# Kernel optimization log

Measured on AMD Instinct MI355X. Metric: run time of the kernel, lower is better.

## Reference

```python
import jax, jax.numpy as jnp
import numpy as np

K = 3       # kernel_size
RATE = 2    # dilation rate
NH = 8      # num_heads
EPS = 1e-5  # InstanceNorm eps


def _conv1x1(x, W, b):
    # x: [B,C,H,W], W: [O,C], b: [O]
    return jnp.einsum('bchw,oc->bohw', x, W) + b[None, :, None, None]


def _inorm(x):
    mu = jnp.mean(x, axis=(2, 3), keepdims=True)
    var = jnp.var(x, axis=(2, 3), keepdims=True)
    return (x - mu) / jnp.sqrt(var + EPS)


def _extract_patches(x):
    # dilated KxK patches, stride 1, 'same' grid -> [B, C, K*K, H, W]
    B, C, H, W = x.shape
    pad = RATE * (K - 1) // 2
    xp = jnp.pad(x, ((0, 0), (0, 0), (pad, pad), (pad, pad)))
    taps = [xp[:, :, i * RATE:i * RATE + H, j * RATE:j * RATE + W]
            for i in range(K) for j in range(K)]
    return jnp.stack(taps, axis=2)


def setup_inputs() -> dict:
    key = jax.random.key(0)
    ks = jax.random.split(key, 8)
    B, C, H, W, A = 1, 64, 64, 64, 128
    features = jax.random.normal(ks[0], (B, C, H, W), jnp.float32)
    masks = jax.random.uniform(ks[1], (B, 1, H, W), jnp.float32)
    s_in = 1.0 / np.sqrt(C).astype(np.float32)
    Wq = jax.random.normal(ks[2], (A, C), jnp.float32) * s_in
    bq = jnp.zeros((A,), jnp.float32)
    Wk = jax.random.normal(ks[3], (A, C), jnp.float32) * s_in
    bk = jnp.zeros((A,), jnp.float32)
    Wo = jax.random.normal(ks[4], (C, C), jnp.float32) * s_in
    bo = jnp.zeros((C,), jnp.float32)
    return dict(features=features, masks=masks, Wq=Wq, bq=bq,
                Wk=Wk, bk=bk, Wo=Wo, bo=bo)


def reference(features, masks, Wq, bq, Wk, bk, Wo, bo):
    B, C, H, W = features.shape
    A = Wq.shape[0]
    hc = A // NH
    L = H * W
    KK = K * K

    m = (masks > 0.5).astype(features.dtype)          # 1 = hole
    f_masked = features * m
    f_unmasked = features * (1.0 - m)

    q = jax.nn.relu(_inorm(_conv1x1(f_masked, Wq, bq)))    # [B,A,H,W]
    k = jax.nn.relu(_inorm(_conv1x1(f_unmasked, Wk, bk)))  # [B,A,H,W]

    # per-head dilated patch banks: [B,NH,hc*KK,L]
    qp = _extract_patches(q).reshape(B, NH, hc * KK, L)
    kp = _extract_patches(k).reshape(B, NH, hc * KK, L)

    # patch-correlation attention per head: [B,NH,L,L]
    attn = jax.nn.softmax(jnp.einsum('bndq,bndk->bnqk', qp, kp), axis=-1)

    # value patch bank from unmasked features: [B,C*KK,L]
    vp = _extract_patches(f_unmasked).reshape(B, C * KK, L)

    # sample value patches: [B,NH,L,C*KK]
    sampled = jnp.einsum('bnqk,bdk->bnqd', attn, vp)

    # fold: average the KK taps per channel, then average over heads
    attended = sampled.reshape(B, NH, L, C, KK).mean(axis=4).mean(axis=1)  # [B,L,C]
    attended = attended.transpose(0, 2, 1).reshape(B, C, H, W)

    return jax.nn.relu(_inorm(_conv1x1(attended, Wo, bo)))
```

## Files before the change

### kernel.cpp

```cpp
#include <hip/hip_runtime.h>
#include <hip/hip_bf16.h>


#define LL 4096
#define CC 64
#define AA 128
#define NH_ 8
#define KSTR 144
#define LOG2E 1.44269504088896340736f

typedef _Float16 half8 __attribute__((ext_vector_type(8)));
typedef float floatx4 __attribute__((ext_vector_type(4)));
typedef int intx4 __attribute__((ext_vector_type(4)));

__device__ __forceinline__ float fexp2(float x) {
    float r;
    asm("v_exp_f32 %0, %1" : "=v"(r) : "v"(x));
    return r;
}

__global__ __launch_bounds__(512) void prep_kernel(
    const float* __restrict__ feat,
    const float* __restrict__ masks,
    const float* __restrict__ Wq, const float* __restrict__ bq,
    const float* __restrict__ Wk, const float* __restrict__ bk,
    _Float16* __restrict__ q_act, _Float16* __restrict__ k_act,
    _Float16* __restrict__ vb)
{
    const int tid = threadIdx.x;
    const int b = blockIdx.x;
    __shared__ float sW[CC];
    __shared__ float sm[16];

    if (b >= 2 * AA) {
        int c = b - 2 * AA;
        for (int p = 0; p < 8; ++p) {
            int l = p * 512 + tid;
            int y = l >> 6, x = l & 63;
            float s = 0.f;
            for (int ty = 0; ty < 3; ++ty) {
                int yy = y + 2 * (ty - 1);
                if (yy < 0 || yy > 63) continue;
                for (int tx = 0; tx < 3; ++tx) {
                    int xx = x + 2 * (tx - 1);
                    if (xx < 0 || xx > 63) continue;
                    int ll = yy * 64 + xx;
                    float hole = masks[ll] > 0.5f ? 1.f : 0.f;
                    s += feat[c * LL + ll] * (1.f - hole);
                }
            }
            vb[c * LL + l] = (_Float16)(s * (1.f / 9.f));
        }
        return;
    }

    const int a = b & (AA - 1);
    const int sel = b >> 7;
    const float* Wrow = (sel ? Wk : Wq) + a * CC;
    const float bias = sel ? bk[a] : bq[a];
    if (tid < CC) sW[tid] = Wrow[tid];
    __syncthreads();

    float acc[8];
#pragma unroll
    for (int p = 0; p < 8; ++p) acc[p] = 0.f;
    for (int c = 0; c < CC; ++c) {
        float wc = sW[c];
        const float* fr = feat + (size_t)c * LL + tid;
#pragma unroll
        for (int p = 0; p < 8; ++p) acc[p] += wc * fr[p * 512];
    }

    float vals[8];
    float s1 = 0.f, s2 = 0.f;
#pragma unroll
    for (int p = 0; p < 8; ++p) {
        int l = p * 512 + tid;
        float hole = masks[l] > 0.5f ? 1.f : 0.f;
        float mf = sel ? (1.f - hole) : hole;
        float v = acc[p] * mf + bias;
        vals[p] = v; s1 += v; s2 += v * v;
    }
    for (int off = 32; off; off >>= 1) {
        s1 += __shfl_down(s1, off, 64);
        s2 += __shfl_down(s2, off, 64);
    }
    int wv = tid >> 6, ln = tid & 63;
    if (ln == 0) { sm[wv * 2] = s1; sm[wv * 2 + 1] = s2; }
    __syncthreads();
    s1 = 0.f; s2 = 0.f;
#pragma unroll
    for (int i = 0; i < 8; ++i) { s1 += sm[2 * i]; s2 += sm[2 * i + 1]; }
    float mu = s1 * (1.f / LL);
    float inv = rsqrtf(s2 * (1.f / LL) - mu * mu + 1e-5f);

    const float oscale = sel ? 1.f : LOG2E;
    _Float16* act = (sel ? k_act : q_act) + (size_t)a * LL;
#pragma unroll
    for (int p = 0; p < 8; ++p) {
        int l = p * 512 + tid;
        float v = (vals[p] - mu) * inv;
        act[l] = (_Float16)(v > 0.f ? v * oscale : 0.f);
    }
}

__global__ __launch_bounds__(256) void build_kp(
    const _Float16* __restrict__ k_act, _Float16* __restrict__ kp)
{
    const int n = blockIdx.x, y = blockIdx.y;
    const int tid = threadIdx.x;
    const _Float16* ka = k_act + (size_t)n * 16 * LL;
    __shared__ _Float16 kt[16][3][72];

    for (int idx = tid; idx < 16 * 3 * 68; idx += 256) {
        int row = idx / 68, xr = idx - row * 68;
        int ah = row / 3, ty = row - ah * 3;
        int yy = y + 2 * (ty - 1);
        int xx = xr - 2;
        _Float16 v = (_Float16)0.f;
        if (yy >= 0 && yy <= 63 && xx >= 0 && xx <= 63)
            v = ka[ah * LL + yy * 64 + xx];
        kt[ah][ty][xr] = v;
    }
    __syncthreads();

    _Float16* base = kp + ((size_t)n * LL + y * 64) * KSTR;
#pragma unroll
    for (int i = 0; i < 5; ++i) {
        int idx = tid + i * 256;
        if (idx < 64 * 18) {
            int x = idx / 18, c18 = idx - x * 18;
            half8 v8;
#pragma unroll
            for (int j = 0; j < 8; ++j) {
                int d = c18 * 8 + j;
                int ah = d / 9, t = d - ah * 9;
                int ty = t / 3, tx = t - ty * 3;
                v8[j] = kt[ah][ty][x + 2 * tx];
            }
            *(half8*)(base + (size_t)idx * 8) = v8;
        }
    }
}

__global__ __launch_bounds__(256, 2) void attn_kernel(
    const _Float16* __restrict__ q_act, const _Float16* __restrict__ kp,
    const _Float16* __restrict__ vb,
    _Float16* __restrict__ Opart, float* __restrict__ ml)
{
    const int bid = blockIdx.x;
    const int n = bid & 7;
    const int slot = bid >> 3;
    const int qt2 = slot & 31;
    const int h = slot >> 5;
    const int jt0 = h * 32;
    const int tid = threadIdx.x;
    const int w = tid >> 6, lane = tid & 63;
    const int l15 = lane & 15, quad = lane >> 4;

    __shared__ __align__(16) _Float16 Bk[2][64 * KSTR + 16];

    if (tid < 32) Bk[tid >> 4][64 * KSTR + (tid & 15)] = (_Float16)0.f;

    const _Float16* kpn = kp + (size_t)n * LL * KSTR;

    auto issue_bk = [&](int jt, _Float16* dst) {
        const char* tile = (const char*)(kpn + (size_t)jt * 64 * KSTR) + (lane << 4);
        for (int c = w; c < 18; c += 4) {
            __builtin_amdgcn_global_load_lds(
                (const __attribute__((address_space(1))) void*)(tile + c * 1024),
                (__attribute__((address_space(3))) void*)(dst + c * 512),
                16, 0, 0);
        }
    };

    half8 afrag[2][5];
    {
        const _Float16* qa = q_act + (size_t)n * 16 * LL;
        const int x = w * 16 + l15;
#pragma unroll
        for (int rs = 0; rs < 2; ++rs) {
            const int y = qt2 * 2 + rs;
#pragma unroll
            for (int ks = 0; ks < 5; ++ks) {
#pragma unroll
                for (int j = 0; j < 8; ++j) {
                    int d = ks * 32 + quad * 8 + j;
                    _Float16 v = (_Float16)0.f;
                    if (d < 144) {
                        int ah = d / 9, t = d - ah * 9;
                        int ty = t / 3, tx = t - ty * 3;
                        int yy = y + 2 * (ty - 1);
                        int xx = x + 2 * (tx - 1);
                        if (yy >= 0 && yy <= 63 && xx >= 0 && xx <= 63)
                            v = qa[ah * LL + yy * 64 + xx];
                    }
                    afrag[rs][ks][j] = v;
                }
            }
        }
    }

    floatx4 accO[2][4];
    float mrow[2], lrow[2];
#pragma unroll
    for (int rs = 0; rs < 2; ++rs) {
        mrow[rs] = -1e30f; lrow[rs] = 0.f;
#pragma unroll
        for (int i = 0; i < 4; ++i) accO[rs][i] = (floatx4){0.f, 0.f, 0.f, 0.f};
    }

    const int aLo = (((quad & 1) << 5) + l15) << 2;
    const int aHi = aLo + 64;
    const bool selHi = (quad >> 1) != 0;

    const _Float16* vpl = vb + (size_t)l15 * LL + quad * 8;

    auto softmax_pack = [&](floatx4* accS, floatx4* accOr,
                            float& mr, float& lr, half8* pfr) {
        float t0 = fmaxf(fmaxf(accS[0][0], accS[0][1]), fmaxf(accS[0][2], accS[0][3]));
        float t1 = fmaxf(fmaxf(accS[1][0], accS[1][1]), fmaxf(accS[1][2], accS[1][3]));
        float t2 = fmaxf(fmaxf(accS[2][0], accS[2][1]), fmaxf(accS[2][2], accS[2][3]));
        float t3 = fmaxf(fmaxf(accS[3][0], accS[3][1]), fmaxf(accS[3][2], accS[3][3]));
        float tm = fmaxf(fmaxf(t0, t1), fmaxf(t2, t3));
        tm = fmaxf(tm, __shfl_xor(tm, 16, 64));
        tm = fmaxf(tm, __shfl_xor(tm, 32, 64));
        float mn = fmaxf(mr, tm);
        float alpha = fexp2(mr - mn);
        mr = mn;
        lr *= alpha;
        float af[4];
#pragma unroll
        for (int r = 0; r < 4; ++r) af[r] = __shfl(alpha, quad * 4 + r, 16);
#pragma unroll
        for (int nt = 0; nt < 4; ++nt)
#pragma unroll
            for (int r = 0; r < 4; ++r) accOr[nt][r] *= af[r];
        float rsum = 0.f;
#pragma unroll
        for (int nt = 0; nt < 4; ++nt)
#pragma unroll
            for (int r = 0; r < 4; ++r) {
                float pv = fexp2(accS[nt][r] - mn);
                accS[nt][r] = pv;
                rsum += pv;
            }
        lr += rsum;

        int pkw[4][2];
#pragma unroll
        for (int nt = 0; nt < 4; ++nt)
#pragma unroll
            for (int rp = 0; rp < 2; ++rp) {
                auto hp = __builtin_amdgcn_cvt_pkrtz(accS[nt][2 * rp],
                                                     accS[nt][2 * rp + 1]);
                pkw[nt][rp] = __builtin_bit_cast(int, hp);
            }
#pragma unroll
        for (int ks2 = 0; ks2 < 2; ++ks2) {
            int w0A = __builtin_amdgcn_ds_bpermute(aLo, pkw[2 * ks2][0]);
            int w0B = __builtin_amdgcn_ds_bpermute(aLo, pkw[2 * ks2 + 1][0]);
            int w1A = __builtin_amdgcn_ds_bpermute(aLo, pkw[2 * ks2][1]);
            int w1B = __builtin_amdgcn_ds_bpermute(aLo, pkw[2 * ks2 + 1][1]);
            int w2A = __builtin_amdgcn_ds_bpermute(aHi, pkw[2 * ks2][0]);
            int w2B = __builtin_amdgcn_ds_bpermute(aHi, pkw[2 * ks2 + 1][0]);
            int w3A = __builtin_amdgcn_ds_bpermute(aHi, pkw[2 * ks2][1]);
            int w3B = __builtin_amdgcn_ds_bpermute(aHi, pkw[2 * ks2 + 1][1]);
            intx4 wvv;
            wvv[0] = selHi ? w0B : w0A;
            wvv[1] = selHi ? w1B : w1A;
            wvv[2] = selHi ? w2B : w2A;
            wvv[3] = selHi ? w3B : w3A;
            pfr[ks2] = __builtin_bit_cast(half8, wvv);
        }
    };

    issue_bk(jt0, Bk[0]);

    int cur = 0;
    for (int it = 0; it < 32; ++it) {
        __syncthreads();

        if (it < 31) issue_bk(jt0 + it + 1, Bk[cur ^ 1]);

        const _Float16* vp = vpl + (jt0 + it) * 64;
        half8 vfrag[4][2];
#pragma unroll
        for (int nt = 0; nt < 4; ++nt)
#pragma unroll
            for (int ks2 = 0; ks2 < 2; ++ks2)
                vfrag[nt][ks2] = *(const half8*)(vp + (size_t)nt * 16 * LL + ks2 * 32);

        const _Float16* bk = Bk[cur];

        floatx4 accS0[4], accS1[4];
#pragma unroll
        for (int i = 0; i < 4; ++i) {
            accS0[i] = (floatx4){0.f, 0.f, 0.f, 0.f};
            accS1[i] = (floatx4){0.f, 0.f, 0.f, 0.f};
        }
        for (int ks = 0; ks < 5; ++ks) {
#pragma unroll
            for (int nt = 0; nt < 4; ++nt) {
                half8 bfr = *(const half8*)(bk + (nt * 16 + l15) * KSTR + ks * 32 + quad * 8);
                accS0[nt] = __builtin_amdgcn_mfma_f32_16x16x32_f16(bfr, afrag[0][ks], accS0[nt], 0, 0, 0);
                accS1[nt] = __builtin_amdgcn_mfma_f32_16x16x32_f16(bfr, afrag[1][ks], accS1[nt], 0, 0, 0);
            }
        }

        half8 pfr0[2], pfr1[2];
        softmax_pack(accS0, accO[0], mrow[0], lrow[0], pfr0);
#pragma unroll
        for (int ks2 = 0; ks2 < 2; ++ks2)
#pragma unroll
            for (int nt = 0; nt < 4; ++nt)
                accO[0][nt] = __builtin_amdgcn_mfma_f32_16x16x32_f16(pfr0[ks2], vfrag[nt][ks2], accO[0][nt], 0, 0, 0);

        softmax_pack(accS1, accO[1], mrow[1], lrow[1], pfr1);
#pragma unroll
        for (int ks2 = 0; ks2 < 2; ++ks2)
#pragma unroll
            for (int nt = 0; nt < 4; ++nt)
                accO[1][nt] = __builtin_amdgcn_mfma_f32_16x16x32_f16(pfr1[ks2], vfrag[nt][ks2], accO[1][nt], 0, 0, 0);

        cur ^= 1;
    }

#pragma unroll
    for (int rs = 0; rs < 2; ++rs) {
        const int y = qt2 * 2 + rs;
        float rsum = lrow[rs];
        rsum += __shfl_xor(rsum, 16, 64);
        rsum += __shfl_xor(rsum, 32, 64);
        float invl = 1.f / rsum;
        float iv[4];
#pragma unroll
        for (int r = 0; r < 4; ++r) iv[r] = __shfl(invl, quad * 4 + r, 16);

        _Float16* op = Opart + ((size_t)(n * 2 + h) * LL + y * 64 + w * 16) * CC;
#pragma unroll
        for (int r = 0; r < 4; ++r)
#pragma unroll
            for (int nt = 0; nt < 4; ++nt)
                op[(quad * 4 + r) * CC + nt * 16 + l15] = (_Float16)(accO[rs][nt][r] * iv[r]);

        if (quad == 0) {
            float* mlp = ml + ((size_t)n * LL + y * 64 + w * 16 + l15) * 4;
            mlp[2 * h] = mrow[rs];
            mlp[2 * h + 1] = rsum;
        }
    }
}

__global__ __launch_bounds__(256) void combine_kernel(
    const _Float16* __restrict__ Opart, const float* __restrict__ ml,
    float* __restrict__ att)
{
    int t = blockIdx.x * 256 + threadIdx.x;
    int l = t >> 6, c = t & 63;
    float s = 0.f;
#pragma unroll
    for (int n = 0; n < NH_; ++n) {
        const float* mlp = ml + ((size_t)n * LL + l) * 4;
        float m0 = mlp[0], l0 = mlp[1], m1 = mlp[2], l1 = mlp[3];
        float M = fmaxf(m0, m1);
        float w0 = l0 * fexp2(m0 - M);
        float w1 = l1 * fexp2(m1 - M);
        float o0 = (float)Opart[((size_t)(2 * n) * LL + l) * CC + c];
        float o1 = (float)Opart[((size_t)(2 * n + 1) * LL + l) * CC + c];
        s += (w0 * o0 + w1 * o1) / (w0 + w1);
    }
    att[t] = s * 0.125f;
}

__global__ __launch_bounds__(1024) void out_kernel(
    const float* __restrict__ att,
    const float* __restrict__ Wo, const float* __restrict__ bo,
    float* __restrict__ out)
{
    const int o = blockIdx.x;
    const int tid = threadIdx.x;
    __shared__ float sW[CC];
    __shared__ float sm[32];
    if (tid < CC) sW[tid] = Wo[o * CC + tid];
    __syncthreads();
    const float bias = bo[o];

    float vals[4], s1 = 0.f, s2 = 0.f;
#pragma unroll
    for (int p = 0; p < 4; ++p) {
        int l = p * 1024 + tid;
        const float4* arow = (const float4*)(att + (size_t)l * CC);
        float acc = bias;
#pragma unroll
        for (int c4 = 0; c4 < 16; ++c4) {
            float4 a4 = arow[c4];
            acc += sW[c4 * 4] * a4.x + sW[c4 * 4 + 1] * a4.y +
                   sW[c4 * 4 + 2] * a4.z + sW[c4 * 4 + 3] * a4.w;
        }
        vals[p] = acc; s1 += acc; s2 += acc * acc;
    }
    for (int off = 32; off; off >>= 1) {
        s1 += __shfl_down(s1, off, 64);
        s2 += __shfl_down(s2, off, 64);
    }
    int wv = tid >> 6, ln = tid & 63;
    if (ln == 0) { sm[wv * 2] = s1; sm[wv * 2 + 1] = s2; }
    __syncthreads();
    s1 = 0.f; s2 = 0.f;
#pragma unroll
    for (int i = 0; i < 16; ++i) { s1 += sm[2 * i]; s2 += sm[2 * i + 1]; }
    float mu = s1 * (1.f / LL);
    float inv = rsqrtf(s2 * (1.f / LL) - mu * mu + 1e-5f);
#pragma unroll
    for (int p = 0; p < 4; ++p) {
        int l = p * 1024 + tid;
        float v = (vals[p] - mu) * inv;
        out[(size_t)o * LL + l] = v > 0.f ? v : 0.f;
    }
}

extern "C" void kernel_launch(void* const* d_in, const int* in_sizes, int n_in,
                              void* d_out, int out_size, void* d_ws, size_t ws_size,
                              hipStream_t stream) {
    const float* feat  = (const float*)d_in[0];
    const float* masks = (const float*)d_in[1];
    const float* Wq    = (const float*)d_in[2];
    const float* bq    = (const float*)d_in[3];
    const float* Wk    = (const float*)d_in[4];
    const float* bk    = (const float*)d_in[5];
    const float* Wo    = (const float*)d_in[6];
    const float* bo    = (const float*)d_in[7];
    float* out = (float*)d_out;

    char* ws = (char*)d_ws;
    _Float16* q_act = (_Float16*)ws;
    _Float16* k_act = (_Float16*)(ws + 1048576);
    _Float16* vb    = (_Float16*)(ws + 2097152);
    float*    att   = (float*)(ws + 2621440);
    _Float16* kp    = (_Float16*)(ws + 3670016);
    _Float16* Opart = (_Float16*)(ws + 13107200);
    float*    ml    = (float*)(ws + 21495808);

    prep_kernel<<<2 * AA + CC, 512, 0, stream>>>(feat, masks, Wq, bq, Wk, bk,
                                                 q_act, k_act, vb);
    dim3 gb(NH_, 64);
    build_kp<<<gb, 256, 0, stream>>>(k_act, kp);
    attn_kernel<<<512, 256, 0, stream>>>(q_act, kp, vb, Opart, ml);
    combine_kernel<<<LL * CC / 256, 256, 0, stream>>>(Opart, ml, att);
    out_kernel<<<CC, 1024, 0, stream>>>(att, Wo, bo, out);
}
```

Before: 228.5 us.

## Process one query row per block to double grid and raise occupancy

The attention kernel now handles a single query row per block instead of two. This halves the register footprint for A fragments, accumulators and softmax state, and raises the launch-bounds occupancy hint from 2 to 4 blocks. The grid doubles to 1024 blocks. In exchange, each K tile loaded into LDS and each V fragment read from global memory is reused by only one row's MFMAs instead of two, which doubles K/V traffic per unit of work.

```diff
diff --git a/kernel.cpp b/kernel.cpp
--- a/kernel.cpp
+++ b/kernel.cpp
@@ -143,16 +143,16 @@
     }
 }
 
-__global__ __launch_bounds__(256, 2) void attn_kernel(
+__global__ __launch_bounds__(256, 4) void attn_kernel(
     const _Float16* __restrict__ q_act, const _Float16* __restrict__ kp,
     const _Float16* __restrict__ vb,
     _Float16* __restrict__ Opart, float* __restrict__ ml)
 {
     const int bid = blockIdx.x;
     const int n = bid & 7;
-    const int slot = bid >> 3;
-    const int qt2 = slot & 31;
-    const int h = slot >> 5;
+    const int rest = bid >> 3;
+    const int qt = rest & 63;
+    const int h = rest >> 6;
     const int jt0 = h * 32;
     const int tid = threadIdx.x;
     const int w = tid >> 6, lane = tid & 63;
@@ -174,41 +174,33 @@
         }
     };
 
-    half8 afrag[2][5];
+    half8 afrag[5];
     {
         const _Float16* qa = q_act + (size_t)n * 16 * LL;
         const int x = w * 16 + l15;
 #pragma unroll
-        for (int rs = 0; rs < 2; ++rs) {
-            const int y = qt2 * 2 + rs;
-#pragma unroll
-            for (int ks = 0; ks < 5; ++ks) {
-#pragma unroll
-                for (int j = 0; j < 8; ++j) {
-                    int d = ks * 32 + quad * 8 + j;
-                    _Float16 v = (_Float16)0.f;
-                    if (d < 144) {
-                        int ah = d / 9, t = d - ah * 9;
-                        int ty = t / 3, tx = t - ty * 3;
-                        int yy = y + 2 * (ty - 1);
-                        int xx = x + 2 * (tx - 1);
-                        if (yy >= 0 && yy <= 63 && xx >= 0 && xx <= 63)
-                            v = qa[ah * LL + yy * 64 + xx];
-                    }
-                    afrag[rs][ks][j] = v;
+        for (int ks = 0; ks < 5; ++ks) {
+#pragma unroll
+            for (int j = 0; j < 8; ++j) {
+                int d = ks * 32 + quad * 8 + j;
+                _Float16 v = (_Float16)0.f;
+                if (d < 144) {
+                    int ah = d / 9, t = d - ah * 9;
+                    int ty = t / 3, tx = t - ty * 3;
+                    int yy = qt + 2 * (ty - 1);
+                    int xx = x + 2 * (tx - 1);
+                    if (yy >= 0 && yy <= 63 && xx >= 0 && xx <= 63)
+                        v = qa[ah * LL + yy * 64 + xx];
                 }
-            }
-        }
-    }
-
-    floatx4 accO[2][4];
-    float mrow[2], lrow[2];
-#pragma unroll
-    for (int rs = 0; rs < 2; ++rs) {
-        mrow[rs] = -1e30f; lrow[rs] = 0.f;
-#pragma unroll
-        for (int i = 0; i < 4; ++i) accO[rs][i] = (floatx4){0.f, 0.f, 0.f, 0.f};
-    }
+                afrag[ks][j] = v;
+            }
+        }
+    }
+
+    floatx4 accO[4];
+    float mrow = -1e30f, lrow = 0.f;
+#pragma unroll
+    for (int i = 0; i < 4; ++i) accO[i] = (floatx4){0.f, 0.f, 0.f, 0.f};
 
     const int aLo = (((quad & 1) << 5) + l15) << 2;
     const int aHi = aLo + 64;
@@ -216,8 +208,35 @@
 
     const _Float16* vpl = vb + (size_t)l15 * LL + quad * 8;
 
-    auto softmax_pack = [&](floatx4* accS, floatx4* accOr,
-                            float& mr, float& lr, half8* pfr) {
+    issue_bk(jt0, Bk[0]);
+
+    int cur = 0;
+    for (int it = 0; it < 32; ++it) {
+        __syncthreads();
+
+        if (it < 31) issue_bk(jt0 + it + 1, Bk[cur ^ 1]);
+
+        const _Float16* vp = vpl + (jt0 + it) * 64;
+        half8 vfrag[4][2];
+#pragma unroll
+        for (int nt = 0; nt < 4; ++nt)
+#pragma unroll
+            for (int ks2 = 0; ks2 < 2; ++ks2)
+                vfrag[nt][ks2] = *(const half8*)(vp + (size_t)nt * 16 * LL + ks2 * 32);
+
+        const _Float16* bk = Bk[cur];
+
+        floatx4 accS[4];
+#pragma unroll
+        for (int i = 0; i < 4; ++i) accS[i] = (floatx4){0.f, 0.f, 0.f, 0.f};
+        for (int ks = 0; ks < 5; ++ks) {
+#pragma unroll
+            for (int nt = 0; nt < 4; ++nt) {
+                half8 bfr = *(const half8*)(bk + (nt * 16 + l15) * KSTR + ks * 32 + quad * 8);
+                accS[nt] = __builtin_amdgcn_mfma_f32_16x16x32_f16(bfr, afrag[ks], accS[nt], 0, 0, 0);
+            }
+        }
+
         float t0 = fmaxf(fmaxf(accS[0][0], accS[0][1]), fmaxf(accS[0][2], accS[0][3]));
         float t1 = fmaxf(fmaxf(accS[1][0], accS[1][1]), fmaxf(accS[1][2], accS[1][3]));
         float t2 = fmaxf(fmaxf(accS[2][0], accS[2][1]), fmaxf(accS[2][2], accS[2][3]));
@@ -225,17 +244,17 @@
         float tm = fmaxf(fmaxf(t0, t1), fmaxf(t2, t3));
         tm = fmaxf(tm, __shfl_xor(tm, 16, 64));
         tm = fmaxf(tm, __shfl_xor(tm, 32, 64));
-        float mn = fmaxf(mr, tm);
-        float alpha = fexp2(mr - mn);
-        mr = mn;
-        lr *= alpha;
+        float mn = fmaxf(mrow, tm);
+        float alpha = fexp2(mrow - mn);
+        mrow = mn;
+        lrow *= alpha;
         float af[4];
 #pragma unroll
         for (int r = 0; r < 4; ++r) af[r] = __shfl(alpha, quad * 4 + r, 16);
 #pragma unroll
         for (int nt = 0; nt < 4; ++nt)
 #pragma unroll
-            for (int r = 0; r < 4; ++r) accOr[nt][r] *= af[r];
+            for (int r = 0; r < 4; ++r) accO[nt][r] *= af[r];
         float rsum = 0.f;
 #pragma unroll
         for (int nt = 0; nt < 4; ++nt)
@@ -245,7 +264,7 @@
                 accS[nt][r] = pv;
                 rsum += pv;
             }
-        lr += rsum;
+        lrow += rsum;
 
         int pkw[4][2];
 #pragma unroll
@@ -256,6 +275,7 @@
                                                      accS[nt][2 * rp + 1]);
                 pkw[nt][rp] = __builtin_bit_cast(int, hp);
             }
+        half8 pfr[2];
 #pragma unroll
         for (int ks2 = 0; ks2 < 2; ++ks2) {
             int w0A = __builtin_amdgcn_ds_bpermute(aLo, pkw[2 * ks2][0]);
@@ -273,63 +293,18 @@
             wvv[3] = selHi ? w3B : w3A;
             pfr[ks2] = __builtin_bit_cast(half8, wvv);
         }
-    };
-
-    issue_bk(jt0, Bk[0]);
-
-    int cur = 0;
-    for (int it = 0; it < 32; ++it) {
-        __syncthreads();
-
-        if (it < 31) issue_bk(jt0 + it + 1, Bk[cur ^ 1]);
-
-        const _Float16* vp = vpl + (jt0 + it) * 64;
-        half8 vfrag[4][2];
-#pragma unroll
-        for (int nt = 0; nt < 4; ++nt)
-#pragma unroll
-            for (int ks2 = 0; ks2 < 2; ++ks2)
-                vfrag[nt][ks2] = *(const half8*)(vp + (size_t)nt * 16 * LL + ks2 * 32);
-
-        const _Float16* bk = Bk[cur];
-
-        floatx4 accS0[4], accS1[4];
-#pragma unroll
-        for (int i = 0; i < 4; ++i) {
-            accS0[i] = (floatx4){0.f, 0.f, 0.f, 0.f};
-            accS1[i] = (floatx4){0.f, 0.f, 0.f, 0.f};
-        }
-        for (int ks = 0; ks < 5; ++ks) {
-#pragma unroll
-            for (int nt = 0; nt < 4; ++nt) {
-                half8 bfr = *(const half8*)(bk + (nt * 16 + l15) * KSTR + ks * 32 + quad * 8);
-                accS0[nt] = __builtin_amdgcn_mfma_f32_16x16x32_f16(bfr, afrag[0][ks], accS0[nt], 0, 0, 0);
-                accS1[nt] = __builtin_amdgcn_mfma_f32_16x16x32_f16(bfr, afrag[1][ks], accS1[nt], 0, 0, 0);
-            }
-        }
-
-        half8 pfr0[2], pfr1[2];
-        softmax_pack(accS0, accO[0], mrow[0], lrow[0], pfr0);
+
 #pragma unroll
         for (int ks2 = 0; ks2 < 2; ++ks2)
 #pragma unroll
             for (int nt = 0; nt < 4; ++nt)
-                accO[0][nt] = __builtin_amdgcn_mfma_f32_16x16x32_f16(pfr0[ks2], vfrag[nt][ks2], accO[0][nt], 0, 0, 0);
-
-        softmax_pack(accS1, accO[1], mrow[1], lrow[1], pfr1);
-#pragma unroll
-        for (int ks2 = 0; ks2 < 2; ++ks2)
-#pragma unroll
-            for (int nt = 0; nt < 4; ++nt)
-                accO[1][nt] = __builtin_amdgcn_mfma_f32_16x16x32_f16(pfr1[ks2], vfrag[nt][ks2], accO[1][nt], 0, 0, 0);
+                accO[nt] = __builtin_amdgcn_mfma_f32_16x16x32_f16(pfr[ks2], vfrag[nt][ks2], accO[nt], 0, 0, 0);
 
         cur ^= 1;
     }
 
-#pragma unroll
-    for (int rs = 0; rs < 2; ++rs) {
-        const int y = qt2 * 2 + rs;
-        float rsum = lrow[rs];
+    {
+        float rsum = lrow;
         rsum += __shfl_xor(rsum, 16, 64);
         rsum += __shfl_xor(rsum, 32, 64);
         float invl = 1.f / rsum;
@@ -337,16 +312,16 @@
 #pragma unroll
         for (int r = 0; r < 4; ++r) iv[r] = __shfl(invl, quad * 4 + r, 16);
 
-        _Float16* op = Opart + ((size_t)(n * 2 + h) * LL + y * 64 + w * 16) * CC;
+        _Float16* op = Opart + ((size_t)(n * 2 + h) * LL + qt * 64 + w * 16) * CC;
 #pragma unroll
         for (int r = 0; r < 4; ++r)
 #pragma unroll
             for (int nt = 0; nt < 4; ++nt)
-                op[(quad * 4 + r) * CC + nt * 16 + l15] = (_Float16)(accO[rs][nt][r] * iv[r]);
+                op[(quad * 4 + r) * CC + nt * 16 + l15] = (_Float16)(accO[nt][r] * iv[r]);
 
         if (quad == 0) {
-            float* mlp = ml + ((size_t)n * LL + y * 64 + w * 16 + l15) * 4;
-            mlp[2 * h] = mrow[rs];
+            float* mlp = ml + ((size_t)n * LL + qt * 64 + w * 16 + l15) * 4;
+            mlp[2 * h] = mrow;
             mlp[2 * h + 1] = rsum;
         }
     }
@@ -446,7 +421,7 @@
                                                  q_act, k_act, vb);
     dim3 gb(NH_, 64);
     build_kp<<<gb, 256, 0, stream>>>(k_act, kp);
-    attn_kernel<<<512, 256, 0, stream>>>(q_act, kp, vb, Opart, ml);
+    attn_kernel<<<1024, 256, 0, stream>>>(q_act, kp, vb, Opart, ml);
     combine_kernel<<<LL * CC / 256, 256, 0, stream>>>(Opart, ml, att);
     out_kernel<<<CC, 1024, 0, stream>>>(att, Wo, bo, out);
 }
```

New measurement: 285.0 us. 1.25x slower.
